# Performance work log

Measured on AMD Instinct MI355X. Metric: run time of the kernel, lower is better.

Reference implementation:

```python
import jax, jax.numpy as jnp
import numpy as np

# Dimensions (see shape_source)
S = 32          # frames
P = 196         # tokens per frame (14x14 patches)
H = 16          # heads
D = 64          # head dim
C = H * D       # 1024
N = S * P       # 6272
B = 1
K_NEAREST = 10
MK = K_NEAREST * P  # max gathered KV tokens per frame (padded)
LN_EPS = 1e-6


def _build_covis_gather(rng):
    """Build [S, MK] gather indices + padding bias from a ragged covisibility mask,
    mirroring SparseAttentionAggregator._build_gather_index."""
    gather_idx = np.zeros((S, MK), dtype=np.int32)
    attn_bias = np.zeros((S, MK), dtype=np.float32)
    arange_p = np.arange(P)
    for i in range(S):
        k_i = int(rng.integers(4, K_NEAREST + 1))  # variable-size covisible set
        others = rng.choice(np.delete(np.arange(S), i), size=k_i - 1, replace=False)
        covis = np.sort(np.concatenate([[i], others]))  # always includes self
        tok = (covis[:, None] * P + arange_p[None, :]).reshape(-1)  # [k_i*P]
        gather_idx[i, : tok.size] = tok
        if tok.size < MK:
            gather_idx[i, tok.size:] = tok[0]   # pad with a valid token
            attn_bias[i, tok.size:] = -1e9      # mask padded positions
    return gather_idx, attn_bias


def setup_inputs() -> dict:
    key = jax.random.key(0)
    kx, kqkv, kproj = jax.random.split(key, 3)
    rng = np.random.default_rng(0)
    gather_idx, attn_bias = _build_covis_gather(rng)
    w_scale = 0.02
    return {
        "x": jax.random.normal(kx, (B, N, C), dtype=jnp.float32),
        "W_qkv": w_scale * jax.random.normal(kqkv, (C, 3 * C), dtype=jnp.float32),
        "b_qkv": jnp.zeros((3 * C,), dtype=jnp.float32),
        "q_gamma": jnp.ones((D,), dtype=jnp.float32),
        "q_beta": jnp.zeros((D,), dtype=jnp.float32),
        "k_gamma": jnp.ones((D,), dtype=jnp.float32),
        "k_beta": jnp.zeros((D,), dtype=jnp.float32),
        "W_proj": w_scale * jax.random.normal(kproj, (C, C), dtype=jnp.float32),
        "b_proj": jnp.zeros((C,), dtype=jnp.float32),
        "gather_idx": jnp.asarray(gather_idx),
        "attn_bias": jnp.asarray(attn_bias),
    }


def _layernorm(t, gamma, beta):
    # LayerNorm over the last (head) dim, as q_norm / k_norm
    mu = jnp.mean(t, axis=-1, keepdims=True)
    var = jnp.mean(jnp.square(t - mu), axis=-1, keepdims=True)
    return (t - mu) * jax.lax.rsqrt(var + LN_EPS) * gamma + beta


def reference(x, W_qkv, b_qkv, q_gamma, q_beta, k_gamma, k_beta, W_proj, b_proj,
              gather_idx, attn_bias):
    Bx, Nx, Cx = x.shape
    mk = gather_idx.shape[1]
    # qkv projection -> q, k, v as [B, H, N, D]
    qkv = (x @ W_qkv + b_qkv).reshape(Bx, Nx, 3, H, D)
    q = jnp.transpose(qkv[:, :, 0], (0, 2, 1, 3))
    k = jnp.transpose(qkv[:, :, 1], (0, 2, 1, 3))
    v = jnp.transpose(qkv[:, :, 2], (0, 2, 1, 3))
    q = _layernorm(q, q_gamma, q_beta)
    k = _layernorm(k, k_gamma, k_beta)
    # single gather of all covisible K/V tokens: [B, H, S*MK, D] -> [B, S, H, MK, D]
    flat_idx = gather_idx.reshape(-1)
    kf = jnp.transpose(k[:, :, flat_idx, :].reshape(Bx, H, S, mk, D), (0, 2, 1, 3, 4))
    vf = jnp.transpose(v[:, :, flat_idx, :].reshape(Bx, H, S, mk, D), (0, 2, 1, 3, 4))
    # queries grouped per frame: [B, S, H, P, D]
    qb = jnp.transpose(q.reshape(Bx, H, S, P, D), (0, 2, 1, 3, 4))
    # batched SDPA over all frames at once
    scores = jnp.einsum('bshpd,bshmd->bshpm', qb, kf) * (D ** -0.5)
    scores = scores + attn_bias[None, :, None, None, :]
    attn = jax.nn.softmax(scores, axis=-1)
    out = jnp.einsum('bshpm,bshmd->bshpd', attn, vf)  # [B, S, H, P, D]
    # back to [B, N, C]
    out = jnp.transpose(out, (0, 2, 1, 3, 4)).reshape(Bx, H, Nx, D)
    out = jnp.transpose(out, (0, 2, 1, 3)).reshape(Bx, Nx, Cx)
    return out @ W_proj + b_proj
```

## Files before the change

kernel.cpp:

```cpp
#include <hip/hip_runtime.h>
#include <hip/hip_bf16.h>
#include <cstdint>
#include <cstddef>

#define S_FRAMES 32
#define P_TOK    196
#define H_HEADS  16
#define D_HEAD   64
#define C_DIM    1024
#define N_TOK    (S_FRAMES * P_TOK)
#define MK_TOK   1960
#define LN_EPS   1e-6f
#define SM_SCALE 0.125f

typedef __attribute__((ext_vector_type(8))) short short8;
typedef __attribute__((ext_vector_type(4))) short short4v;
typedef __attribute__((ext_vector_type(4))) float f32x4;

static __device__ __forceinline__ ushort f2bf(float x) {
  union { float f; unsigned u; } c; c.f = x;
  unsigned r = (c.u + 0x7FFFu + ((c.u >> 16) & 1u)) >> 16;
  return (ushort)r;
}
static __device__ __forceinline__ float bf2f(ushort h) {
  union { unsigned u; float f; } c; c.u = ((unsigned)h) << 16;
  return c.f;
}
static __device__ __forceinline__ unsigned pack_bf16x2(float a, float b) {
  union { float f; unsigned u; } x, y; x.f = a; y.f = b;
  unsigned lo = (x.u + 0x7FFFu + ((x.u >> 16) & 1u)) >> 16;
  unsigned hi = (y.u + 0x7FFFu + ((y.u >> 16) & 1u)) >> 16;
  return lo | (hi << 16);
}

__global__ __launch_bounds__(256) void wsplit_kernel(
    const float* __restrict__ W, ushort* __restrict__ Bth,
    ushort* __restrict__ Btl, int K, int Nn)
{
  __shared__ float T[64][72];
  const int n0 = blockIdx.x * 64;
  const int k0 = blockIdx.y * 64;
  const int tid = threadIdx.x;

  for (int idx = tid; idx < 64 * 16; idx += 256) {
    int r = idx >> 4, c4 = idx & 15;
    *(float4*)&T[r][c4 * 4] = *(const float4*)(W + (size_t)(k0 + r) * Nn + n0 + c4 * 4);
  }
  __syncthreads();
  for (int idx = tid; idx < 64 * 8; idx += 256) {
    int nr = idx >> 3, ch = idx & 7;
    short8 hi, lo;
    #pragma unroll
    for (int u = 0; u < 8; ++u) {
      float v = T[ch * 8 + u][nr];
      ushort h = f2bf(v);
      hi[u] = (short)h;
      lo[u] = (short)f2bf(v - bf2f(h));
    }
    *(short8*)(Bth + (size_t)(n0 + nr) * K + k0 + ch * 8) = hi;
    *(short8*)(Btl + (size_t)(n0 + nr) * K + k0 + ch * 8) = lo;
  }
}

template <int AMODE, int EMODE>
__global__ __launch_bounds__(256, 2) void gemm_split3(
    const void* __restrict__ Ap, const void* __restrict__ Ap2,
    const ushort* __restrict__ Bth, const ushort* __restrict__ Btl,
    const float* __restrict__ bias, float* __restrict__ Cout,
    ushort* __restrict__ Qb, ushort* __restrict__ Kb, ushort* __restrict__ Vtg,
    const float* __restrict__ qg, const float* __restrict__ qbet,
    const float* __restrict__ kg, const float* __restrict__ kbet,
    int M, int Nn, int K)
{
  __shared__ ushort Ah[128 * 64];
  __shared__ ushort Al[128 * 64];
  __shared__ ushort Bh[128 * 64];
  __shared__ ushort Bl[128 * 64];

  const int tid  = threadIdx.x;
  const int wave = tid >> 6;
  const int lane = tid & 63;
  const int g    = lane >> 4;
  const int lq   = lane & 15;
  const int bm   = blockIdx.y * 128;
  const int bn   = blockIdx.x * 128;
  const int wm   = (wave >> 1) * 64;
  const int wn   = (wave & 1) * 64;

  f32x4 acc[4][4];
  #pragma unroll
  for (int i = 0; i < 4; ++i)
    #pragma unroll
    for (int j = 0; j < 4; ++j) {
      acc[i][j][0] = 0.f; acc[i][j][1] = 0.f;
      acc[i][j][2] = 0.f; acc[i][j][3] = 0.f;
    }

  for (int k0 = 0; k0 < K; k0 += 64) {
    __syncthreads();
    for (int idx = tid; idx < 128 * 8; idx += 256) {
      const int row = idx >> 3, c = idx & 7;
      const int gc = c ^ (row & 7);
      if (AMODE == 0) {
        const float* ap = (const float*)Ap + (size_t)(bm + row) * K + k0 + gc * 8;
        float4 f0 = *(const float4*)ap;
        float4 f1 = *(const float4*)(ap + 4);
        float v[8] = {f0.x, f0.y, f0.z, f0.w, f1.x, f1.y, f1.z, f1.w};
        short8 hi, lo;
        #pragma unroll
        for (int u = 0; u < 8; ++u) {
          ushort h = f2bf(v[u]);
          hi[u] = (short)h;
          lo[u] = (short)f2bf(v[u] - bf2f(h));
        }
        *(short8*)&Ah[row * 64 + c * 8] = hi;
        *(short8*)&Al[row * 64 + c * 8] = lo;
      } else {
        *(short8*)&Ah[row * 64 + c * 8] =
            *(const short8*)((const ushort*)Ap  + (size_t)(bm + row) * K + k0 + gc * 8);
        *(short8*)&Al[row * 64 + c * 8] =
            *(const short8*)((const ushort*)Ap2 + (size_t)(bm + row) * K + k0 + gc * 8);
      }
      *(short8*)&Bh[row * 64 + c * 8] =
          *(const short8*)(Bth + (size_t)(bn + row) * K + k0 + gc * 8);
      *(short8*)&Bl[row * 64 + c * 8] =
          *(const short8*)(Btl + (size_t)(bn + row) * K + k0 + gc * 8);
    }
    __syncthreads();

    #pragma unroll
    for (int kt = 0; kt < 2; ++kt) {
      short8 ah[4], al[4], bh[4], bl[4];
      #pragma unroll
      for (int mi = 0; mi < 4; ++mi) {
        const int row = wm + mi * 16 + lq;
        const int sl = (kt * 4 + g) ^ (row & 7);
        ah[mi] = *(const short8*)&Ah[row * 64 + sl * 8];
        al[mi] = *(const short8*)&Al[row * 64 + sl * 8];
      }
      #pragma unroll
      for (int ni = 0; ni < 4; ++ni) {
        const int row = wn + ni * 16 + lq;
        const int sl = (kt * 4 + g) ^ (row & 7);
        bh[ni] = *(const short8*)&Bh[row * 64 + sl * 8];
        bl[ni] = *(const short8*)&Bl[row * 64 + sl * 8];
      }
      #pragma unroll
      for (int mi = 0; mi < 4; ++mi)
        #pragma unroll
        for (int ni = 0; ni < 4; ++ni) {
          acc[mi][ni] = __builtin_amdgcn_mfma_f32_16x16x32_bf16(ah[mi], bl[ni], acc[mi][ni], 0, 0, 0);
          acc[mi][ni] = __builtin_amdgcn_mfma_f32_16x16x32_bf16(al[mi], bh[ni], acc[mi][ni], 0, 0, 0);
          acc[mi][ni] = __builtin_amdgcn_mfma_f32_16x16x32_bf16(ah[mi], bh[ni], acc[mi][ni], 0, 0, 0);
        }
    }
  }

  const int col0 = bn + wn;
  float bias4[4];
  #pragma unroll
  for (int ni = 0; ni < 4; ++ni) bias4[ni] = bias[col0 + ni * 16 + lq];

  if (EMODE == 0) {
    #pragma unroll
    for (int mi = 0; mi < 4; ++mi)
      #pragma unroll
      for (int r = 0; r < 4; ++r) {
        float* cp = Cout + (size_t)(bm + wm + mi * 16 + g * 4 + r) * Nn + col0;
        #pragma unroll
        for (int ni = 0; ni < 4; ++ni)
          cp[ni * 16 + lq] = acc[mi][ni][r] + bias4[ni];
      }
  } else {
    const int type = col0 >> 10;
    const int h    = (col0 & 1023) >> 6;
    if (type < 2) {
      const float* gam = type ? kg : qg;
      const float* bet = type ? kbet : qbet;
      float gm[4], bt[4];
      #pragma unroll
      for (int ni = 0; ni < 4; ++ni) {
        gm[ni] = gam[ni * 16 + lq];
        bt[ni] = bet[ni * 16 + lq];
      }
      ushort* outb = (type ? Kb : Qb);
      #pragma unroll
      for (int mi = 0; mi < 4; ++mi)
        #pragma unroll
        for (int r = 0; r < 4; ++r) {
          float xv[4];
          float s = 0.f;
          #pragma unroll
          for (int ni = 0; ni < 4; ++ni) {
            xv[ni] = acc[mi][ni][r] + bias4[ni];
            s += xv[ni];
          }
          s += __shfl_xor(s, 1, 64);
          s += __shfl_xor(s, 2, 64);
          s += __shfl_xor(s, 4, 64);
          s += __shfl_xor(s, 8, 64);
          const float mu = s * (1.0f / 64.0f);
          float ss = 0.f;
          #pragma unroll
          for (int ni = 0; ni < 4; ++ni) {
            float dd = xv[ni] - mu;
            ss += dd * dd;
          }
          ss += __shfl_xor(ss, 1, 64);
          ss += __shfl_xor(ss, 2, 64);
          ss += __shfl_xor(ss, 4, 64);
          ss += __shfl_xor(ss, 8, 64);
          const float rs = rsqrtf(ss * (1.0f / 64.0f) + LN_EPS);
          const int tok = bm + wm + mi * 16 + g * 4 + r;
          ushort* op = outb + ((size_t)h * N_TOK + tok) * 64;
          #pragma unroll
          for (int ni = 0; ni < 4; ++ni)
            op[ni * 16 + lq] = f2bf((xv[ni] - mu) * rs * gm[ni] + bt[ni]);
        }
    } else {
      #pragma unroll
      for (int mi = 0; mi < 4; ++mi) {
        const int tok = bm + wm + mi * 16 + g * 4;
        #pragma unroll
        for (int ni = 0; ni < 4; ++ni) {
          const int d = ni * 16 + lq;
          short4v w;
          #pragma unroll
          for (int r = 0; r < 4; ++r) w[r] = (short)f2bf(acc[mi][ni][r] + bias4[ni]);
          *(short4v*)&Vtg[((size_t)(h * 64 + d)) * N_TOK + tok] = w;
        }
      }
    }
  }
}

__global__ __launch_bounds__(512, 2) void attn_mfma_kernel(
    const ushort* __restrict__ Qb, const ushort* __restrict__ Kb,
    const ushort* __restrict__ Vtg,
    const int* __restrict__ gather_idx, const float* __restrict__ attn_bias,
    ushort* __restrict__ Chi, ushort* __restrict__ Clo)
{
  constexpr int KROWS = 224;
  constexpr int VROW  = 232;
  constexpr int PROW  = 40;
  __shared__ ushort Ks[KROWS * 64];
  __shared__ ushort Vs[64 * VROW];
  __shared__ ushort Pl[8][16 * PROW];

  const int s = blockIdx.x >> 4;
  const int h = blockIdx.x & 15;
  const int tid = threadIdx.x;
  const int wave = tid >> 6;
  const int lane = tid & 63;
  const int g  = lane >> 4;
  const int lq = lane & 15;
  const int nq = (wave < 5) ? 2 : 1;

  const float KEXP = 0.18033688011112042f;
  const float BEXP = 11.541560327111708f;

  for (int c = tid; c < (KROWS - P_TOK) * 8; c += 512) {
    const int row = P_TOK + (c >> 3), ch = c & 7;
    short8 z = {0,0,0,0,0,0,0,0};
    *(short8*)&Ks[row * 64 + (ch << 3)] = z;
  }
  for (int c = tid; c < 64 * 7; c += 512) {
    const int d = c / 7, ch = 49 + (c % 7);
    short4v z = {0,0,0,0};
    *(short4v*)&Vs[d * VROW + (ch << 2)] = z;
  }

  f32x4 oacc[2][4];
  #pragma unroll
  for (int t = 0; t < 2; ++t)
    #pragma unroll
    for (int dt = 0; dt < 4; ++dt) {
      oacc[t][dt][0] = 0.f; oacc[t][dt][1] = 0.f;
      oacc[t][dt][2] = 0.f; oacc[t][dt][3] = 0.f;
    }
  float lsum[2] = {0.f, 0.f};

  for (int f = 0; f < 10; ++f) {
    if (attn_bias[(size_t)s * MK_TOK + f * P_TOK] < -1.0e8f) break;
    const int tok0 = gather_idx[(size_t)s * MK_TOK + f * P_TOK];
    __syncthreads();

    for (int c = tid; c < P_TOK * 8; c += 512) {
      const int row = c >> 3, ch = c & 7;
      *(short8*)&Ks[row * 64 + ((ch ^ (row & 7)) << 3)] =
          *(const short8*)(Kb + ((size_t)h * N_TOK + tok0 + row) * 64 + (ch << 3));
    }
    for (int c = tid; c < 64 * 49; c += 512) {
      const int d = c / 49, ch = c - d * 49;
      *(short4v*)&Vs[d * VROW + (ch << 2)] =
          *(const short4v*)(Vtg + ((size_t)(h * 64 + d)) * N_TOK + tok0 + (ch << 2));
    }
    __syncthreads();

    #pragma unroll
    for (int t = 0; t < 2; ++t) {
      if (t >= nq) break;
      const int qt = wave + t * 8;
      int qrow = qt * 16 + lq; if (qrow > P_TOK - 1) qrow = P_TOK - 1;
      const ushort* qbase = Qb + ((size_t)h * N_TOK + s * P_TOK + qrow) * 64 + g * 8;
      const short8 qf0 = *(const short8*)(qbase);
      const short8 qf1 = *(const short8*)(qbase + 32);

      for (int kt2 = 0; kt2 < 7; ++kt2) {
        #pragma unroll
        for (int half = 0; half < 2; ++half) {
          const int kt = kt2 * 2 + half;
          f32x4 sacc = {0.f, 0.f, 0.f, 0.f};
          if (kt < 13) {
            const int row = kt * 16 + lq;
            const int sw = row & 7;
            short8 ka0 = *(const short8*)&Ks[row * 64 + ((g ^ sw) << 3)];
            short8 ka1 = *(const short8*)&Ks[row * 64 + (((4 + g) ^ sw) << 3)];
            sacc = __builtin_amdgcn_mfma_f32_16x16x32_bf16(ka0, qf0, sacc, 0, 0, 0);
            sacc = __builtin_amdgcn_mfma_f32_16x16x32_bf16(ka1, qf1, sacc, 0, 0, 0);
          }
          float p[4];
          #pragma unroll
          for (int r = 0; r < 4; ++r) {
            const int kv = kt * 16 + g * 4 + r;
            float e = __builtin_exp2f(fmaf(sacc[r], KEXP, -BEXP));
            p[r] = (kv < P_TOK) ? e : 0.f;
            lsum[t] += p[r];
          }
          ushort* pw = &Pl[wave][lq * PROW + half * 16 + g * 4];
          *(unsigned*)(pw)     = pack_bf16x2(p[0], p[1]);
          *(unsigned*)(pw + 2) = pack_bf16x2(p[2], p[3]);
        }
        const short8 pa = *(const short8*)&Pl[wave][lq * PROW + g * 8];
        #pragma unroll
        for (int dt = 0; dt < 4; ++dt) {
          const short8 vb = *(const short8*)&Vs[(dt * 16 + lq) * VROW + kt2 * 32 + g * 8];
          oacc[t][dt] = __builtin_amdgcn_mfma_f32_16x16x32_bf16(pa, vb, oacc[t][dt], 0, 0, 0);
        }
      }
    }
  }

  #pragma unroll
  for (int t = 0; t < 2; ++t) {
    if (t >= nq) break;
    const int qt = wave + t * 8;
    float lv = lsum[t];
    lv += __shfl_xor(lv, 16, 64);
    lv += __shfl_xor(lv, 32, 64);
    #pragma unroll
    for (int r = 0; r < 4; ++r) {
      const int qrow = qt * 16 + g * 4 + r;
      const float lr = __shfl(lv, (lane & 48) | (g * 4 + r), 64);
      const float inv = 1.0f / lr;
      if (qrow < P_TOK) {
        const size_t rowb = ((size_t)(s * P_TOK + qrow)) * C_DIM + h * 64;
        #pragma unroll
        for (int dt = 0; dt < 4; ++dt) {
          float val = oacc[t][dt][r] * inv;
          ushort hi = f2bf(val);
          Chi[rowb + dt * 16 + lq] = hi;
          Clo[rowb + dt * 16 + lq] = f2bf(val - bf2f(hi));
        }
      }
    }
  }
}

__global__ __launch_bounds__(256) void sgemm_bias_kernel(
    const float* __restrict__ A, const float* __restrict__ B,
    const float* __restrict__ bias, float* __restrict__ C,
    int M, int N, int K)
{
  constexpr int BM = 64, BN = 64, BK = 16;
  __shared__ alignas(16) float As[BK][BM + 4];
  __shared__ alignas(16) float Bs[BK][BN + 4];

  const int tid = threadIdx.x;
  const int bm = blockIdx.y * BM;
  const int bn = blockIdx.x * BN;
  const int tx = tid & 15;
  const int ty = tid >> 4;
  const int ar = tid >> 2;
  const int ak = (tid & 3) * 4;
  const int br = tid >> 4;
  const int bc = (tid & 15) * 4;

  float acc[4][4] = {};

  for (int k0 = 0; k0 < K; k0 += BK) {
    __syncthreads();
    float4 av = *(const float4*)(A + (size_t)(bm + ar) * K + k0 + ak);
    As[ak + 0][ar] = av.x;
    As[ak + 1][ar] = av.y;
    As[ak + 2][ar] = av.z;
    As[ak + 3][ar] = av.w;
    *(float4*)&Bs[br][bc] = *(const float4*)(B + (size_t)(k0 + br) * N + bn + bc);
    __syncthreads();

    #pragma unroll
    for (int kk = 0; kk < BK; ++kk) {
      float4 a4 = *(const float4*)&As[kk][ty * 4];
      float4 b4 = *(const float4*)&Bs[kk][tx * 4];
      float aa[4] = {a4.x, a4.y, a4.z, a4.w};
      float bb[4] = {b4.x, b4.y, b4.z, b4.w};
      #pragma unroll
      for (int i = 0; i < 4; ++i)
        #pragma unroll
        for (int j = 0; j < 4; ++j)
          acc[i][j] = fmaf(aa[i], bb[j], acc[i][j]);
    }
  }

  #pragma unroll
  for (int i = 0; i < 4; ++i) {
    float4 o;
    o.x = acc[i][0] + bias[bn + tx * 4 + 0];
    o.y = acc[i][1] + bias[bn + tx * 4 + 1];
    o.z = acc[i][2] + bias[bn + tx * 4 + 2];
    o.w = acc[i][3] + bias[bn + tx * 4 + 3];
    *(float4*)(C + (size_t)(bm + ty * 4 + i) * N + bn + tx * 4) = o;
  }
}

__global__ __launch_bounds__(128) void qk_ln_kernel(
    float* __restrict__ qkv,
    const float* __restrict__ qg, const float* __restrict__ qb,
    const float* __restrict__ kg, const float* __restrict__ kb)
{
  const int r = blockIdx.x;
  const int n = r / H_HEADS;
  const int h = r % H_HEADS;
  const int wave = threadIdx.x >> 6;
  const int lane = threadIdx.x & 63;

  float* p = qkv + (size_t)n * (3 * C_DIM) + wave * C_DIM + h * D_HEAD + lane;
  float v = *p;
  float sum = v;
  #pragma unroll
  for (int off = 32; off; off >>= 1) sum += __shfl_xor(sum, off, 64);
  float mu = sum * (1.0f / 64.0f);
  float d = v - mu;
  float vs = d * d;
  #pragma unroll
  for (int off = 32; off; off >>= 1) vs += __shfl_xor(vs, off, 64);
  float var = vs * (1.0f / 64.0f);
  float rstd = rsqrtf(var + LN_EPS);
  const float* gg = wave ? kg : qg;
  const float* bb = wave ? kb : qb;
  *p = d * rstd * gg[lane] + bb[lane];
}

__global__ __launch_bounds__(256) void sparse_attn_kernel(
    const float* __restrict__ qkv,
    const int*   __restrict__ gather_idx,
    const float* __restrict__ attn_bias,
    float* __restrict__ attn_out)
{
  constexpr int KC = 64;
  __shared__ alignas(16) float Ksf[KC][D_HEAD + 4];
  __shared__ alignas(16) float Vsf[KC][D_HEAD + 4];
  __shared__ float biasS[KC];

  const int s = blockIdx.x >> 4;
  const int h = blockIdx.x & 15;
  const int tid = threadIdx.x;
  const int p = tid;
  const bool active = (p < P_TOK);

  const int*   gi = gather_idx + (size_t)s * MK_TOK;
  const float* bi = attn_bias + (size_t)s * MK_TOK;

  const int qrow = s * P_TOK + (active ? p : 0);
  const float* qptr = qkv + (size_t)qrow * (3 * C_DIM) + h * D_HEAD;
  float q[D_HEAD];
  #pragma unroll
  for (int c = 0; c < 16; ++c) {
    float4 t4 = *(const float4*)(qptr + 4 * c);
    q[4 * c + 0] = t4.x; q[4 * c + 1] = t4.y;
    q[4 * c + 2] = t4.z; q[4 * c + 3] = t4.w;
  }

  float m = -3.0e38f;
  float l = 0.0f;
  float acc[D_HEAD] = {};
  const int jld = tid & 63;
  const int cpart = tid >> 6;

  for (int j0 = 0; j0 < MK_TOK; j0 += KC) {
    const int jn = min(KC, MK_TOK - j0);
    __syncthreads();
    if (jld < jn) {
      const int idx = gi[j0 + jld];
      const float* kbp = qkv + (size_t)idx * (3 * C_DIM) + C_DIM + h * D_HEAD + cpart * 16;
      const float* vbp = kbp + C_DIM;
      #pragma unroll
      for (int u = 0; u < 4; ++u) {
        *(float4*)&Ksf[jld][cpart * 16 + 4 * u] = *(const float4*)(kbp + 4 * u);
        *(float4*)&Vsf[jld][cpart * 16 + 4 * u] = *(const float4*)(vbp + 4 * u);
      }
    }
    if (tid < jn) biasS[tid] = bi[j0 + tid];
    __syncthreads();

    for (int j = 0; j < jn; ++j) {
      float s0 = 0.f, s1 = 0.f, s2 = 0.f, s3 = 0.f;
      #pragma unroll
      for (int c = 0; c < 16; ++c) {
        float4 kv = *(const float4*)&Ksf[j][4 * c];
        s0 = fmaf(q[4 * c + 0], kv.x, s0);
        s1 = fmaf(q[4 * c + 1], kv.y, s1);
        s2 = fmaf(q[4 * c + 2], kv.z, s2);
        s3 = fmaf(q[4 * c + 3], kv.w, s3);
      }
      float sc = (s0 + s1) + (s2 + s3);
      sc = sc * SM_SCALE + biasS[j];
      if (sc > m) {
        float al = __expf(m - sc);
        l *= al;
        #pragma unroll
        for (int d = 0; d < D_HEAD; ++d) acc[d] *= al;
        m = sc;
      }
      float pe = __expf(sc - m);
      l += pe;
      #pragma unroll
      for (int c = 0; c < 16; ++c) {
        float4 vv = *(const float4*)&Vsf[j][4 * c];
        acc[4 * c + 0] = fmaf(pe, vv.x, acc[4 * c + 0]);
        acc[4 * c + 1] = fmaf(pe, vv.y, acc[4 * c + 1]);
        acc[4 * c + 2] = fmaf(pe, vv.z, acc[4 * c + 2]);
        acc[4 * c + 3] = fmaf(pe, vv.w, acc[4 * c + 3]);
      }
    }
  }

  if (active) {
    const float inv = 1.0f / l;
    float* op = attn_out + (size_t)(s * P_TOK + p) * C_DIM + h * D_HEAD;
    #pragma unroll
    for (int c = 0; c < 16; ++c) {
      float4 o;
      o.x = acc[4 * c + 0] * inv;
      o.y = acc[4 * c + 1] * inv;
      o.z = acc[4 * c + 2] * inv;
      o.w = acc[4 * c + 3] * inv;
      *(float4*)(op + 4 * c) = o;
    }
  }
}

extern "C" void kernel_launch(void* const* d_in, const int* in_sizes, int n_in,
                              void* d_out, int out_size, void* d_ws, size_t ws_size,
                              hipStream_t stream)
{
  const float* x      = (const float*)d_in[0];
  const float* W_qkv  = (const float*)d_in[1];
  const float* b_qkv  = (const float*)d_in[2];
  const float* q_g    = (const float*)d_in[3];
  const float* q_b    = (const float*)d_in[4];
  const float* k_g    = (const float*)d_in[5];
  const float* k_b    = (const float*)d_in[6];
  const float* W_proj = (const float*)d_in[7];
  const float* b_proj = (const float*)d_in[8];
  const int*   g_idx  = (const int*)d_in[9];
  const float* a_bias = (const float*)d_in[10];
  float* out = (float*)d_out;

  const size_t VS = (size_t)H_HEADS * D_HEAD * N_TOK;
  const size_t WQ = (size_t)3 * C_DIM * C_DIM;
  const size_t WP = (size_t)C_DIM * C_DIM;
  const size_t need_new = (5 * VS + 2 * WQ + 2 * WP) * sizeof(ushort);

  if (ws_size >= need_new) {
    ushort* base = (ushort*)d_ws;
    ushort* Vtg  = base;
    ushort* Qb   = base + VS;
    ushort* Kb   = base + 2 * VS;
    ushort* Chi  = base + 3 * VS;
    ushort* Clo  = base + 4 * VS;
    ushort* WqT_h = base + 5 * VS;
    ushort* WqT_l = WqT_h + WQ;
    ushort* WpT_h = WqT_l + WQ;
    ushort* WpT_l = WpT_h + WP;

    wsplit_kernel<<<dim3(48, 16), 256, 0, stream>>>(W_qkv, WqT_h, WqT_l, C_DIM, 3 * C_DIM);
    wsplit_kernel<<<dim3(16, 16), 256, 0, stream>>>(W_proj, WpT_h, WpT_l, C_DIM, C_DIM);

    gemm_split3<0, 1><<<dim3(24, 49), 256, 0, stream>>>(
        x, nullptr, WqT_h, WqT_l, b_qkv, nullptr,
        Qb, Kb, Vtg, q_g, q_b, k_g, k_b, N_TOK, 3 * C_DIM, C_DIM);

    attn_mfma_kernel<<<S_FRAMES * H_HEADS, 512, 0, stream>>>(
        Qb, Kb, Vtg, g_idx, a_bias, Chi, Clo);

    gemm_split3<1, 0><<<dim3(8, 49), 256, 0, stream>>>(
        Chi, Clo, WpT_h, WpT_l, b_proj, out,
        nullptr, nullptr, nullptr, nullptr, nullptr, nullptr, nullptr,
        N_TOK, C_DIM, C_DIM);
  } else {
    float* qkv      = (float*)d_ws;
    float* attn_out = qkv + (size_t)N_TOK * 3 * C_DIM;
    sgemm_bias_kernel<<<dim3((3 * C_DIM) / 64, N_TOK / 64), 256, 0, stream>>>(
        x, W_qkv, b_qkv, qkv, N_TOK, 3 * C_DIM, C_DIM);
    qk_ln_kernel<<<N_TOK * H_HEADS, 128, 0, stream>>>(qkv, q_g, q_b, k_g, k_b);
    sparse_attn_kernel<<<S_FRAMES * H_HEADS, 256, 0, stream>>>(
        qkv, g_idx, a_bias, attn_out);
    sgemm_bias_kernel<<<dim3(C_DIM / 64, N_TOK / 64), 256, 0, stream>>>(
        attn_out, W_proj, b_proj, out, N_TOK, C_DIM, C_DIM);
  }
}
```

Measured before the change: 503.3 us.

## Pre-split x to bf16 hi/lo and stage GEMM tiles via direct global-to-LDS loads

Adds a separate kernel that converts x into bf16 hi/lo planes once, so the QKV GEMM no longer repeats the fp32 split for every N-tile column block. Both GEMMs now load A and B tiles with global_load_lds (16-byte direct-to-LDS copies) using precomputed swizzled offsets, which avoids staging the data through registers. The cost is an extra pass over x and extra workspace traffic, and the LDS layout now depends on the per-lane address mapping matching the old swizzle.

```diff
diff --git a/kernel.cpp b/kernel.cpp
--- a/kernel.cpp
+++ b/kernel.cpp
@@ -33,6 +33,10 @@
   return lo | (hi << 16);
 }
 
+#define GLOAD16(g, l) __builtin_amdgcn_global_load_lds( \
+    (const __attribute__((address_space(1))) void*)(g), \
+    (__attribute__((address_space(3))) void*)(l), 16, 0, 0)
+
 __global__ __launch_bounds__(256) void wsplit_kernel(
     const float* __restrict__ W, ushort* __restrict__ Bth,
     ushort* __restrict__ Btl, int K, int Nn)
@@ -62,9 +66,28 @@
   }
 }
 
-template <int AMODE, int EMODE>
+__global__ __launch_bounds__(256) void xsplit_kernel(
+    const float* __restrict__ x, ushort* __restrict__ Xh,
+    ushort* __restrict__ Xl, int n4)
+{
+  for (int i = blockIdx.x * 256 + threadIdx.x; i < n4; i += gridDim.x * 256) {
+    float4 v = ((const float4*)x)[i];
+    float vv[4] = {v.x, v.y, v.z, v.w};
+    short4v h, lo;
+    #pragma unroll
+    for (int u = 0; u < 4; ++u) {
+      ushort hb = f2bf(vv[u]);
+      h[u] = (short)hb;
+      lo[u] = (short)f2bf(vv[u] - bf2f(hb));
+    }
+    ((short4v*)Xh)[i] = h;
+    ((short4v*)Xl)[i] = lo;
+  }
+}
+
+template <int EMODE>
 __global__ __launch_bounds__(256, 2) void gemm_split3(
-    const void* __restrict__ Ap, const void* __restrict__ Ap2,
+    const ushort* __restrict__ Ah_g, const ushort* __restrict__ Al_g,
     const ushort* __restrict__ Bth, const ushort* __restrict__ Btl,
     const float* __restrict__ bias, float* __restrict__ Cout,
     ushort* __restrict__ Qb, ushort* __restrict__ Kb, ushort* __restrict__ Vtg,
@@ -87,6 +110,17 @@
   const int wm   = (wave >> 1) * 64;
   const int wn   = (wave & 1) * 64;
 
+  size_t offA[4], offB[4];
+  unsigned ldsoff[4];
+  #pragma unroll
+  for (int i = 0; i < 4; ++i) {
+    const int tr = wave * 8 + i * 32 + (lane >> 3);
+    const int gc = (lane & 7) ^ (tr & 7);
+    offA[i] = (size_t)(bm + tr) * K + gc * 8;
+    offB[i] = (size_t)(bn + tr) * K + gc * 8;
+    ldsoff[i] = (unsigned)(wave * 512 + i * 2048);
+  }
+
   f32x4 acc[4][4];
   #pragma unroll
   for (int i = 0; i < 4; ++i)
@@ -98,33 +132,12 @@
 
   for (int k0 = 0; k0 < K; k0 += 64) {
     __syncthreads();
-    for (int idx = tid; idx < 128 * 8; idx += 256) {
-      const int row = idx >> 3, c = idx & 7;
-      const int gc = c ^ (row & 7);
-      if (AMODE == 0) {
-        const float* ap = (const float*)Ap + (size_t)(bm + row) * K + k0 + gc * 8;
-        float4 f0 = *(const float4*)ap;
-        float4 f1 = *(const float4*)(ap + 4);
-        float v[8] = {f0.x, f0.y, f0.z, f0.w, f1.x, f1.y, f1.z, f1.w};
-        short8 hi, lo;
-        #pragma unroll
-        for (int u = 0; u < 8; ++u) {
-          ushort h = f2bf(v[u]);
-          hi[u] = (short)h;
-          lo[u] = (short)f2bf(v[u] - bf2f(h));
-        }
-        *(short8*)&Ah[row * 64 + c * 8] = hi;
-        *(short8*)&Al[row * 64 + c * 8] = lo;
-      } else {
-        *(short8*)&Ah[row * 64 + c * 8] =
-            *(const short8*)((const ushort*)Ap  + (size_t)(bm + row) * K + k0 + gc * 8);
-        *(short8*)&Al[row * 64 + c * 8] =
-            *(const short8*)((const ushort*)Ap2 + (size_t)(bm + row) * K + k0 + gc * 8);
-      }
-      *(short8*)&Bh[row * 64 + c * 8] =
-          *(const short8*)(Bth + (size_t)(bn + row) * K + k0 + gc * 8);
-      *(short8*)&Bl[row * 64 + c * 8] =
-          *(const short8*)(Btl + (size_t)(bn + row) * K + k0 + gc * 8);
+    #pragma unroll
+    for (int i = 0; i < 4; ++i) {
+      GLOAD16(Ah_g + offA[i] + k0, &Ah[ldsoff[i]]);
+      GLOAD16(Al_g + offA[i] + k0, &Al[ldsoff[i]]);
+      GLOAD16(Bth  + offB[i] + k0, &Bh[ldsoff[i]]);
+      GLOAD16(Btl  + offB[i] + k0, &Bl[ldsoff[i]]);
     }
     __syncthreads();
 
@@ -583,18 +596,21 @@
     ushort* WqT_l = WqT_h + WQ;
     ushort* WpT_h = WqT_l + WQ;
     ushort* WpT_l = WpT_h + WP;
+    ushort* Xh = Chi;
+    ushort* Xl = Clo;
 
     wsplit_kernel<<<dim3(48, 16), 256, 0, stream>>>(W_qkv, WqT_h, WqT_l, C_DIM, 3 * C_DIM);
     wsplit_kernel<<<dim3(16, 16), 256, 0, stream>>>(W_proj, WpT_h, WpT_l, C_DIM, C_DIM);
-
-    gemm_split3<0, 1><<<dim3(24, 49), 256, 0, stream>>>(
-        x, nullptr, WqT_h, WqT_l, b_qkv, nullptr,
+    xsplit_kernel<<<2048, 256, 0, stream>>>(x, Xh, Xl, N_TOK * C_DIM / 4);
+
+    gemm_split3<1><<<dim3(24, 49), 256, 0, stream>>>(
+        Xh, Xl, WqT_h, WqT_l, b_qkv, nullptr,
         Qb, Kb, Vtg, q_g, q_b, k_g, k_b, N_TOK, 3 * C_DIM, C_DIM);
 
     attn_mfma_kernel<<<S_FRAMES * H_HEADS, 512, 0, stream>>>(
         Qb, Kb, Vtg, g_idx, a_bias, Chi, Clo);
 
-    gemm_split3<1, 0><<<dim3(8, 49), 256, 0, stream>>>(
+    gemm_split3<0><<<dim3(8, 49), 256, 0, stream>>>(
         Chi, Clo, WpT_h, WpT_l, b_proj, out,
         nullptr, nullptr, nullptr, nullptr, nullptr, nullptr, nullptr,
         N_TOK, C_DIM, C_DIM);
```

Measured after the change: 436.1 us. 13.4% less time.
